# Performance work log

Measured on AMD Instinct MI355X. Metric: run time of the kernel, lower is better.

The kernel has to match this reference:

```python
import jax, jax.numpy as jnp
import numpy as np

N_NODES = 50000
N_EDGES = 800000
IN_DIM = 128
HID_DIM = 64


def gcn_conv(x, W, b, src, dst, ew):
    """PyG GCNConv with edge_weight: add self-loops (weight 1), symmetric
    normalization D^-1/2 (A+I) D^-1/2, linear transform, scatter-add, bias."""
    n = x.shape[0]
    loop = jnp.arange(n)
    src_a = jnp.concatenate([src, loop])           # [E+N]
    dst_a = jnp.concatenate([dst, loop])
    ew_a = jnp.concatenate([ew, jnp.ones((n,), dtype=x.dtype)])
    deg = jax.ops.segment_sum(ew_a, dst_a, num_segments=n)   # [N]
    dinv = jnp.where(deg > 0, jax.lax.rsqrt(deg), 0.0)
    norm = dinv[src_a] * ew_a * dinv[dst_a]        # [E+N]
    h = x @ W                                      # [N, out]
    msg = h[src_a] * norm[:, None]                 # gather + scale
    out = jax.ops.segment_sum(msg, dst_a, num_segments=n)    # scatter-add
    return out + b


def setup_inputs() -> dict:
    key = jax.random.key(0)
    k = jax.random.split(key, 6)
    x = jax.random.normal(k[0], (N_NODES, IN_DIM), dtype=jnp.float32)
    edge_index = jax.random.randint(k[1], (2, N_EDGES), 0, N_NODES, dtype=jnp.int64)
    edge_weight = jax.random.uniform(k[2], (N_EDGES,), dtype=jnp.float32)
    W1 = jax.random.normal(k[3], (IN_DIM, HID_DIM), dtype=jnp.float32) * (1.0 / np.sqrt(IN_DIM))
    b1 = jnp.zeros((HID_DIM,), dtype=jnp.float32)
    W2 = jax.random.normal(k[4], (HID_DIM, 1), dtype=jnp.float32) * (1.0 / np.sqrt(HID_DIM))
    b2 = jnp.zeros((1,), dtype=jnp.float32)
    return {"x": x, "edge_index": edge_index, "edge_weight": edge_weight,
            "W1": W1, "b1": b1, "W2": W2, "b2": b2}


def reference(x, edge_index, edge_weight, W1, b1, W2, b2):
    src, dst = edge_index[0], edge_index[1]
    h = gcn_conv(x, W1, b1, src, dst, edge_weight)
    h = jax.nn.relu(h)
    h = gcn_conv(h, W2, b2, src, dst, edge_weight)
    return jax.nn.sigmoid(h).squeeze(-1)           # [N]
```

## Files before the change

### kernel.cpp

```cpp
#include <hip/hip_runtime.h>
#include <hip/hip_bf16.h>
#include <math.h>

#define N_NODES 50000
#define N_EDGES 800000
#define IN_DIM  128
#define HID_DIM 64

#define NBKT     196
#define BKT_CAP  5000
#define NPASSC   200
#define EDGES_PER_PASSC (N_EDGES / NPASSC)
#define GEMM_NODES 64
#define NGEMM    782
#define XS_LD    132

__global__ __launch_bounds__(256)
void partgemm_kernel(const int* __restrict__ src, const int* __restrict__ dst,
                     const float* __restrict__ ew, int* __restrict__ gcursor,
                     int2* __restrict__ edge_b,
                     const float* __restrict__ x, const float* __restrict__ W1,
                     __hip_bfloat16* __restrict__ h1b) {
    __shared__ float w1s[IN_DIM * HID_DIM];
    __shared__ float xs[GEMM_NODES][XS_LD];
    int bid = blockIdx.x;
    int tid = threadIdx.x;
    if (bid < NPASSC) {
        int* cnt1    = (int*)w1s;
        int* cnt2    = cnt1 + NBKT;
        int* runbase = cnt2 + NBKT;
        if (tid < NBKT) { cnt1[tid] = 0; cnt2[tid] = 0; }
        __syncthreads();
        int e0 = bid * EDGES_PER_PASSC;
        for (int i = tid; i < EDGES_PER_PASSC; i += 256)
            atomicAdd(&cnt1[dst[e0 + i] >> 8], 1);
        __syncthreads();
        if (tid < NBKT) {
            int c = cnt1[tid];
            runbase[tid] = (c > 0) ? atomicAdd(&gcursor[tid], c) : 0;
        }
        __syncthreads();
        for (int i = tid; i < EDGES_PER_PASSC; i += 256) {
            int e = e0 + i;
            int d = dst[e];
            int b = d >> 8;
            int lr = atomicAdd(&cnt2[b], 1);
            int pos = b * BKT_CAP + runbase[b] + lr;
            edge_b[pos] = make_int2(src[e] | ((d & 255) << 16), __float_as_int(ew[e]));
        }
        return;
    }
    int gb = bid - NPASSC;
    int node0 = gb * GEMM_NODES;
    const float4* W4 = (const float4*)W1;
    float4* w1s4 = (float4*)w1s;
#pragma unroll
    for (int i = 0; i < 8; ++i) w1s4[tid + 256 * i] = W4[tid + 256 * i];
    {
        int r = tid >> 2, q = tid & 3;
        int row = node0 + r;
        if (row >= N_NODES) row = N_NODES - 1;
        const float4* xr = (const float4*)(x + (long)row * IN_DIM + q * 32);
#pragma unroll
        for (int i = 0; i < 8; ++i)
            *(float4*)&xs[r][q * 32 + i * 4] = xr[i];
    }
    __syncthreads();
    int w    = tid >> 6;
    int lane = tid & 63;
    int ng   = lane >> 2;
    int jg   = lane & 3;
    int j0   = w * 16 + jg * 4;
    float acc[4][4] = {{0.f}};
#pragma unroll 2
    for (int k = 0; k < IN_DIM; k += 4) {
        float4 wr0 = *(const float4*)&w1s[(k + 0) * HID_DIM + j0];
        float4 wr1 = *(const float4*)&w1s[(k + 1) * HID_DIM + j0];
        float4 wr2 = *(const float4*)&w1s[(k + 2) * HID_DIM + j0];
        float4 wr3 = *(const float4*)&w1s[(k + 3) * HID_DIM + j0];
#pragma unroll
        for (int i = 0; i < 4; ++i) {
            float4 xv = *(const float4*)&xs[ng + 16 * i][k];
            acc[i][0] += xv.x * wr0.x + xv.y * wr1.x + xv.z * wr2.x + xv.w * wr3.x;
            acc[i][1] += xv.x * wr0.y + xv.y * wr1.y + xv.z * wr2.y + xv.w * wr3.y;
            acc[i][2] += xv.x * wr0.z + xv.y * wr1.z + xv.z * wr2.z + xv.w * wr3.z;
            acc[i][3] += xv.x * wr0.w + xv.y * wr1.w + xv.z * wr2.w + xv.w * wr3.w;
        }
    }
#pragma unroll
    for (int i = 0; i < 4; ++i) {
        int n = node0 + ng + 16 * i;
        if (n < N_NODES) {
            __hip_bfloat16 bf[4];
            bf[0] = __float2bfloat16(acc[i][0]);
            bf[1] = __float2bfloat16(acc[i][1]);
            bf[2] = __float2bfloat16(acc[i][2]);
            bf[3] = __float2bfloat16(acc[i][3]);
            *(uint2*)&h1b[(long)n * HID_DIM + j0] = *(uint2*)bf;
        }
    }
}

__global__ __launch_bounds__(1024)
void bsort_kernel(const int* __restrict__ gcursor, const int2* __restrict__ edge_b,
                  int2* __restrict__ edge_s, int* __restrict__ start_g,
                  int* __restrict__ cnt_g, float* __restrict__ dinv) {
    __shared__ int   cnt[256];
    __shared__ int   cnt2[256];
    __shared__ float deg[256];
    __shared__ int   sc[256];
    int b   = blockIdx.x;
    int tid = threadIdx.x;
    int M    = gcursor[b];
    int base = b * BKT_CAP;
    if (tid < 256) { cnt[tid] = 0; cnt2[tid] = 0; deg[tid] = 0.0f; }
    __syncthreads();
    for (int i = tid; i < M; i += 1024) {
        int2 e = edge_b[base + i];
        int ld = (e.x >> 16) & 255;
        atomicAdd(&cnt[ld], 1);
        atomicAdd(&deg[ld], __int_as_float(e.y));
    }
    __syncthreads();
    if (tid < 256) sc[tid] = cnt[tid];
    __syncthreads();
#pragma unroll
    for (int off = 1; off < 256; off <<= 1) {
        int t = (tid >= off && tid < 256) ? sc[tid - off] : 0;
        __syncthreads();
        if (tid < 256) sc[tid] += t;
        __syncthreads();
    }
    if (tid < 256) {
        int startL = sc[tid] - cnt[tid];
        int node = b * 256 + tid;
        if (node < N_NODES) {
            start_g[node] = base + startL;
            cnt_g[node]   = cnt[tid];
            dinv[node]    = rsqrtf(1.0f + deg[tid]);
        }
        sc[tid] = startL;
    }
    __syncthreads();
    for (int i = tid; i < M; i += 1024) {
        int2 e = edge_b[base + i];
        int ld = (e.x >> 16) & 255;
        int r = atomicAdd(&cnt2[ld], 1);
        edge_s[base + sc[ld] + r] = make_int2(e.x & 0xFFFF, e.y);
    }
}

__global__ void gather1_layer2_kernel(const int* __restrict__ start_g, const int* __restrict__ cnt_g,
                                      const int2* __restrict__ edge_s,
                                      const __hip_bfloat16* __restrict__ h1b,
                                      const float* __restrict__ dinv, const float* __restrict__ b1,
                                      const float* __restrict__ W2, float* __restrict__ h2s) {
    __shared__ int2 meta[4][64];
    int wave = (blockIdx.x * blockDim.x + threadIdx.x) >> 6;
    int wl = threadIdx.x >> 6;
    int lane = threadIdx.x & 63;
    if (wave >= N_NODES) return;
    int s0 = start_g[wave];
    int ctotal = cnt_g[wave];
    int c0 = (lane & 31) * 2;
    int half = lane >> 5;
    float accA = 0.f, accB = 0.f;
    float accA2 = 0.f, accB2 = 0.f;
    for (int done = 0; done < ctotal; done += 64) {
        int cnt = ctotal - done;
        if (cnt > 64) cnt = 64;
        if (lane < cnt) {
            int2 m = edge_s[s0 + done + lane];
            float w = __int_as_float(m.y) * dinv[m.x];
            meta[wl][lane] = make_int2(m.x, __float_as_int(w));
        }
        __builtin_amdgcn_wave_barrier();
        int cnte = cnt & ~1;
        int j = 0;
        for (; j + 16 <= cnte; j += 16) {
            int2 m0 = meta[wl][j +  0 + half];
            int2 m1 = meta[wl][j +  2 + half];
            int2 m2 = meta[wl][j +  4 + half];
            int2 m3 = meta[wl][j +  6 + half];
            int2 m4 = meta[wl][j +  8 + half];
            int2 m5 = meta[wl][j + 10 + half];
            int2 m6 = meta[wl][j + 12 + half];
            int2 m7 = meta[wl][j + 14 + half];
            unsigned int p0 = *(const unsigned int*)&h1b[m0.x * HID_DIM + c0];
            unsigned int p1 = *(const unsigned int*)&h1b[m1.x * HID_DIM + c0];
            unsigned int p2 = *(const unsigned int*)&h1b[m2.x * HID_DIM + c0];
            unsigned int p3 = *(const unsigned int*)&h1b[m3.x * HID_DIM + c0];
            unsigned int p4 = *(const unsigned int*)&h1b[m4.x * HID_DIM + c0];
            unsigned int p5 = *(const unsigned int*)&h1b[m5.x * HID_DIM + c0];
            unsigned int p6 = *(const unsigned int*)&h1b[m6.x * HID_DIM + c0];
            unsigned int p7 = *(const unsigned int*)&h1b[m7.x * HID_DIM + c0];
            float w0 = __int_as_float(m0.y), w1 = __int_as_float(m1.y);
            float w2 = __int_as_float(m2.y), w3 = __int_as_float(m3.y);
            float w4 = __int_as_float(m4.y), w5 = __int_as_float(m5.y);
            float w6 = __int_as_float(m6.y), w7 = __int_as_float(m7.y);
            accA  += w0 * __uint_as_float(p0 << 16);
            accB  += w0 * __uint_as_float(p0 & 0xFFFF0000u);
            accA2 += w1 * __uint_as_float(p1 << 16);
            accB2 += w1 * __uint_as_float(p1 & 0xFFFF0000u);
            accA  += w2 * __uint_as_float(p2 << 16);
            accB  += w2 * __uint_as_float(p2 & 0xFFFF0000u);
            accA2 += w3 * __uint_as_float(p3 << 16);
            accB2 += w3 * __uint_as_float(p3 & 0xFFFF0000u);
            accA  += w4 * __uint_as_float(p4 << 16);
            accB  += w4 * __uint_as_float(p4 & 0xFFFF0000u);
            accA2 += w5 * __uint_as_float(p5 << 16);
            accB2 += w5 * __uint_as_float(p5 & 0xFFFF0000u);
            accA  += w6 * __uint_as_float(p6 << 16);
            accB  += w6 * __uint_as_float(p6 & 0xFFFF0000u);
            accA2 += w7 * __uint_as_float(p7 << 16);
            accB2 += w7 * __uint_as_float(p7 & 0xFFFF0000u);
        }
        for (; j + 2 <= cnte; j += 2) {
            int2 m = meta[wl][j + half];
            unsigned int p = *(const unsigned int*)&h1b[m.x * HID_DIM + c0];
            accA += __int_as_float(m.y) * __uint_as_float(p << 16);
            accB += __int_as_float(m.y) * __uint_as_float(p & 0xFFFF0000u);
        }
        if (cnt & 1) {
            if (half == 0) {
                int2 m = meta[wl][cnt - 1];
                unsigned int p = *(const unsigned int*)&h1b[m.x * HID_DIM + c0];
                accA += __int_as_float(m.y) * __uint_as_float(p << 16);
                accB += __int_as_float(m.y) * __uint_as_float(p & 0xFFFF0000u);
            }
        }
        __builtin_amdgcn_wave_barrier();
    }
    accA += accA2; accB += accB2;
    accA += __shfl_xor(accA, 32, 64);
    accB += __shfl_xor(accB, 32, 64);
    float di = dinv[wave];
    unsigned int sp = *(const unsigned int*)&h1b[wave * HID_DIM + c0];
    float s0f = __uint_as_float(sp << 16);
    float s1f = __uint_as_float(sp & 0xFFFF0000u);
    float z0 = di * (accA + di * s0f) + b1[c0];
    float z1 = di * (accB + di * s1f) + b1[c0 + 1];
    float h0 = fmaxf(z0, 0.0f);
    float h1v = fmaxf(z1, 0.0f);
    float v = h0 * W2[c0] + h1v * W2[c0 + 1];
#pragma unroll
    for (int off = 16; off > 0; off >>= 1)
        v += __shfl_down(v, off, 32);
    if (lane == 0) h2s[wave] = v * di;
}

__global__ void gather2_final_kernel(const int* __restrict__ start_g, const int* __restrict__ cnt_g,
                                     const int2* __restrict__ edge_s,
                                     const float* __restrict__ h2s, const float* __restrict__ dinv,
                                     const float* __restrict__ b2, float* __restrict__ out) {
    int t = blockIdx.x * blockDim.x + threadIdx.x;
    int n = t >> 4;
    int sub = t & 15;
    if (n >= N_NODES) return;
    int s0 = start_g[n];
    int cnt = cnt_g[n];
    float acc = 0.0f;
    for (int j = sub; j < cnt; j += 16) {
        int2 m = edge_s[s0 + j];
        acc += __int_as_float(m.y) * h2s[m.x];
    }
#pragma unroll
    for (int off = 8; off > 0; off >>= 1)
        acc += __shfl_down(acc, off, 16);
    if (sub == 0) {
        float z = dinv[n] * (acc + h2s[n]) + b2[0];
        out[n] = 1.0f / (1.0f + expf(-z));
    }
}

extern "C" void kernel_launch(void* const* d_in, const int* in_sizes, int n_in,
                              void* d_out, int out_size, void* d_ws, size_t ws_size,
                              hipStream_t stream) {
    const float* x  = (const float*)d_in[0];
    const int*   ei = (const int*)d_in[1];
    const float* ew = (const float*)d_in[2];
    const float* W1 = (const float*)d_in[3];
    const float* b1 = (const float*)d_in[4];
    const float* W2 = (const float*)d_in[5];
    const float* b2 = (const float*)d_in[6];
    float* out = (float*)d_out;

    const int* src = ei;
    const int* dst = ei + N_EDGES;

    char* ws = (char*)d_ws;
    int2*  edge_b  = (int2*)ws;              ws += (size_t)NBKT * BKT_CAP * sizeof(int2);
    int2*  edge_s  = (int2*)ws;              ws += (size_t)NBKT * BKT_CAP * sizeof(int2);
    int*   gcursor = (int*)ws;               ws += NBKT * sizeof(int);
    int*   start_g = (int*)ws;               ws += N_NODES * sizeof(int);
    int*   cnt_g   = (int*)ws;               ws += N_NODES * sizeof(int);
    float* dinv    = (float*)ws;             ws += N_NODES * sizeof(float);
    float* h2s     = (float*)ws;             ws += N_NODES * sizeof(float);
    ws = (char*)(((uintptr_t)ws + 127) & ~(uintptr_t)127);
    __hip_bfloat16* h1b = (__hip_bfloat16*)ws;

    hipMemsetAsync(gcursor, 0, NBKT * sizeof(int), stream);
    partgemm_kernel<<<NPASSC + NGEMM, 256, 0, stream>>>(src, dst, ew, gcursor, edge_b, x, W1, h1b);
    bsort_kernel<<<NBKT, 1024, 0, stream>>>(gcursor, edge_b, edge_s, start_g, cnt_g, dinv);
    gather1_layer2_kernel<<<(N_NODES * 64) / 256, 256, 0, stream>>>(start_g, cnt_g, edge_s, h1b, dinv, b1, W2, h2s);
    gather2_final_kernel<<<(N_NODES * 16 + 255) / 256, 256, 0, stream>>>(start_g, cnt_g, edge_s, h2s, dinv, b2, out);
}
```

Measured before the change: 155.1 us.

## Fuse bucket sort and both gathers into one cooperative persistent kernel

Replaces three kernel launches (bucket sort, layer-1 gather plus layer-2 transform, final gather) with one cooperative kernel that separates the phases with grid-wide syncs. The grid is persistent and capped by occupancy, so gather work is distributed with grid-stride loops. The aim is to remove launch gaps and kernel-boundary drains. In exchange the sort phase now runs with 256 threads per block instead of 1024, grid syncs add their own cost, and the fixed grid of 1024 blocks may give lower parallelism for the gather phases than the former large launches.

New measurement: 376.8 us. 143% more time.

```diff
diff --git a/kernel.cpp b/kernel.cpp
--- a/kernel.cpp
+++ b/kernel.cpp
@@ -1,6 +1,9 @@
 #include <hip/hip_runtime.h>
 #include <hip/hip_bf16.h>
+#include <hip/hip_cooperative_groups.h>
 #include <math.h>
+
+namespace cg = cooperative_groups;
 
 #define N_NODES 50000
 #define N_EDGES 800000
@@ -14,6 +17,7 @@
 #define GEMM_NODES 64
 #define NGEMM    782
 #define XS_LD    132
+#define GRID_FUSED 1024
 
 __global__ __launch_bounds__(256)
 void partgemm_kernel(const int* __restrict__ src, const int* __restrict__ dst,
@@ -101,175 +105,175 @@
     }
 }
 
-__global__ __launch_bounds__(1024)
-void bsort_kernel(const int* __restrict__ gcursor, const int2* __restrict__ edge_b,
-                  int2* __restrict__ edge_s, int* __restrict__ start_g,
-                  int* __restrict__ cnt_g, float* __restrict__ dinv) {
+__global__ __launch_bounds__(256, 4)
+void fused_post_kernel(const int* __restrict__ gcursor, const int2* __restrict__ edge_b,
+                       int2* __restrict__ edge_s, int* __restrict__ start_g,
+                       int* __restrict__ cnt_g, float* __restrict__ dinv,
+                       const __hip_bfloat16* __restrict__ h1b,
+                       const float* __restrict__ b1, const float* __restrict__ W2,
+                       float* __restrict__ h2s, const float* __restrict__ b2,
+                       float* __restrict__ out) {
+    cg::grid_group grid = cg::this_grid();
     __shared__ int   cnt[256];
     __shared__ int   cnt2[256];
     __shared__ float deg[256];
     __shared__ int   sc[256];
-    int b   = blockIdx.x;
+    __shared__ int2  meta[4][64];
     int tid = threadIdx.x;
-    int M    = gcursor[b];
-    int base = b * BKT_CAP;
-    if (tid < 256) { cnt[tid] = 0; cnt2[tid] = 0; deg[tid] = 0.0f; }
-    __syncthreads();
-    for (int i = tid; i < M; i += 1024) {
-        int2 e = edge_b[base + i];
-        int ld = (e.x >> 16) & 255;
-        atomicAdd(&cnt[ld], 1);
-        atomicAdd(&deg[ld], __int_as_float(e.y));
-    }
-    __syncthreads();
-    if (tid < 256) sc[tid] = cnt[tid];
-    __syncthreads();
-#pragma unroll
-    for (int off = 1; off < 256; off <<= 1) {
-        int t = (tid >= off && tid < 256) ? sc[tid - off] : 0;
-        __syncthreads();
-        if (tid < 256) sc[tid] += t;
-        __syncthreads();
-    }
-    if (tid < 256) {
+    int bid = blockIdx.x;
+    int gthread  = bid * 256 + tid;
+    int nthreads = gridDim.x * 256;
+
+    if (bid < NBKT) {
+        int M    = gcursor[bid];
+        int base = bid * BKT_CAP;
+        cnt[tid] = 0; cnt2[tid] = 0; deg[tid] = 0.0f;
+        __syncthreads();
+        for (int i = tid; i < M; i += 256) {
+            int2 e = edge_b[base + i];
+            int ld = (e.x >> 16) & 255;
+            atomicAdd(&cnt[ld], 1);
+            atomicAdd(&deg[ld], __int_as_float(e.y));
+        }
+        __syncthreads();
+        sc[tid] = cnt[tid];
+        __syncthreads();
+#pragma unroll
+        for (int off = 1; off < 256; off <<= 1) {
+            int t = (tid >= off) ? sc[tid - off] : 0;
+            __syncthreads();
+            sc[tid] += t;
+            __syncthreads();
+        }
         int startL = sc[tid] - cnt[tid];
-        int node = b * 256 + tid;
+        int node = bid * 256 + tid;
         if (node < N_NODES) {
             start_g[node] = base + startL;
             cnt_g[node]   = cnt[tid];
             dinv[node]    = rsqrtf(1.0f + deg[tid]);
         }
         sc[tid] = startL;
-    }
-    __syncthreads();
-    for (int i = tid; i < M; i += 1024) {
-        int2 e = edge_b[base + i];
-        int ld = (e.x >> 16) & 255;
-        int r = atomicAdd(&cnt2[ld], 1);
-        edge_s[base + sc[ld] + r] = make_int2(e.x & 0xFFFF, e.y);
-    }
-}
-
-__global__ void gather1_layer2_kernel(const int* __restrict__ start_g, const int* __restrict__ cnt_g,
-                                      const int2* __restrict__ edge_s,
-                                      const __hip_bfloat16* __restrict__ h1b,
-                                      const float* __restrict__ dinv, const float* __restrict__ b1,
-                                      const float* __restrict__ W2, float* __restrict__ h2s) {
-    __shared__ int2 meta[4][64];
-    int wave = (blockIdx.x * blockDim.x + threadIdx.x) >> 6;
-    int wl = threadIdx.x >> 6;
-    int lane = threadIdx.x & 63;
-    if (wave >= N_NODES) return;
-    int s0 = start_g[wave];
-    int ctotal = cnt_g[wave];
-    int c0 = (lane & 31) * 2;
-    int half = lane >> 5;
-    float accA = 0.f, accB = 0.f;
-    float accA2 = 0.f, accB2 = 0.f;
-    for (int done = 0; done < ctotal; done += 64) {
-        int cnt = ctotal - done;
-        if (cnt > 64) cnt = 64;
-        if (lane < cnt) {
-            int2 m = edge_s[s0 + done + lane];
-            float w = __int_as_float(m.y) * dinv[m.x];
-            meta[wl][lane] = make_int2(m.x, __float_as_int(w));
-        }
-        __builtin_amdgcn_wave_barrier();
-        int cnte = cnt & ~1;
-        int j = 0;
-        for (; j + 16 <= cnte; j += 16) {
-            int2 m0 = meta[wl][j +  0 + half];
-            int2 m1 = meta[wl][j +  2 + half];
-            int2 m2 = meta[wl][j +  4 + half];
-            int2 m3 = meta[wl][j +  6 + half];
-            int2 m4 = meta[wl][j +  8 + half];
-            int2 m5 = meta[wl][j + 10 + half];
-            int2 m6 = meta[wl][j + 12 + half];
-            int2 m7 = meta[wl][j + 14 + half];
-            unsigned int p0 = *(const unsigned int*)&h1b[m0.x * HID_DIM + c0];
-            unsigned int p1 = *(const unsigned int*)&h1b[m1.x * HID_DIM + c0];
-            unsigned int p2 = *(const unsigned int*)&h1b[m2.x * HID_DIM + c0];
-            unsigned int p3 = *(const unsigned int*)&h1b[m3.x * HID_DIM + c0];
-            unsigned int p4 = *(const unsigned int*)&h1b[m4.x * HID_DIM + c0];
-            unsigned int p5 = *(const unsigned int*)&h1b[m5.x * HID_DIM + c0];
-            unsigned int p6 = *(const unsigned int*)&h1b[m6.x * HID_DIM + c0];
-            unsigned int p7 = *(const unsigned int*)&h1b[m7.x * HID_DIM + c0];
-            float w0 = __int_as_float(m0.y), w1 = __int_as_float(m1.y);
-            float w2 = __int_as_float(m2.y), w3 = __int_as_float(m3.y);
-            float w4 = __int_as_float(m4.y), w5 = __int_as_float(m5.y);
-            float w6 = __int_as_float(m6.y), w7 = __int_as_float(m7.y);
-            accA  += w0 * __uint_as_float(p0 << 16);
-            accB  += w0 * __uint_as_float(p0 & 0xFFFF0000u);
-            accA2 += w1 * __uint_as_float(p1 << 16);
-            accB2 += w1 * __uint_as_float(p1 & 0xFFFF0000u);
-            accA  += w2 * __uint_as_float(p2 << 16);
-            accB  += w2 * __uint_as_float(p2 & 0xFFFF0000u);
-            accA2 += w3 * __uint_as_float(p3 << 16);
-            accB2 += w3 * __uint_as_float(p3 & 0xFFFF0000u);
-            accA  += w4 * __uint_as_float(p4 << 16);
-            accB  += w4 * __uint_as_float(p4 & 0xFFFF0000u);
-            accA2 += w5 * __uint_as_float(p5 << 16);
-            accB2 += w5 * __uint_as_float(p5 & 0xFFFF0000u);
-            accA  += w6 * __uint_as_float(p6 << 16);
-            accB  += w6 * __uint_as_float(p6 & 0xFFFF0000u);
-            accA2 += w7 * __uint_as_float(p7 << 16);
-            accB2 += w7 * __uint_as_float(p7 & 0xFFFF0000u);
-        }
-        for (; j + 2 <= cnte; j += 2) {
-            int2 m = meta[wl][j + half];
-            unsigned int p = *(const unsigned int*)&h1b[m.x * HID_DIM + c0];
-            accA += __int_as_float(m.y) * __uint_as_float(p << 16);
-            accB += __int_as_float(m.y) * __uint_as_float(p & 0xFFFF0000u);
-        }
-        if (cnt & 1) {
-            if (half == 0) {
-                int2 m = meta[wl][cnt - 1];
-                unsigned int p = *(const unsigned int*)&h1b[m.x * HID_DIM + c0];
-                accA += __int_as_float(m.y) * __uint_as_float(p << 16);
-                accB += __int_as_float(m.y) * __uint_as_float(p & 0xFFFF0000u);
+        __syncthreads();
+        for (int i = tid; i < M; i += 256) {
+            int2 e = edge_b[base + i];
+            int ld = (e.x >> 16) & 255;
+            int r = atomicAdd(&cnt2[ld], 1);
+            edge_s[base + sc[ld] + r] = make_int2(e.x & 0xFFFF, e.y);
+        }
+    }
+    grid.sync();
+
+    {
+        int wl   = tid >> 6;
+        int lane = tid & 63;
+        int gwave    = gthread >> 6;
+        int totWaves = nthreads >> 6;
+        int c0   = (lane & 31) * 2;
+        int half = lane >> 5;
+        for (int node = gwave; node < N_NODES; node += totWaves) {
+            int s0 = start_g[node];
+            int ctotal = cnt_g[node];
+            float accA = 0.f, accB = 0.f, accA2 = 0.f, accB2 = 0.f;
+            for (int done = 0; done < ctotal; done += 64) {
+                int cnt_ = ctotal - done;
+                if (cnt_ > 64) cnt_ = 64;
+                if (lane < cnt_) {
+                    int2 m = edge_s[s0 + done + lane];
+                    float w = __int_as_float(m.y) * dinv[m.x];
+                    meta[wl][lane] = make_int2(m.x, __float_as_int(w));
+                }
+                __builtin_amdgcn_wave_barrier();
+                int cnte = cnt_ & ~1;
+                int j = 0;
+                for (; j + 16 <= cnte; j += 16) {
+                    int2 m0 = meta[wl][j +  0 + half];
+                    int2 m1 = meta[wl][j +  2 + half];
+                    int2 m2 = meta[wl][j +  4 + half];
+                    int2 m3 = meta[wl][j +  6 + half];
+                    int2 m4 = meta[wl][j +  8 + half];
+                    int2 m5 = meta[wl][j + 10 + half];
+                    int2 m6 = meta[wl][j + 12 + half];
+                    int2 m7 = meta[wl][j + 14 + half];
+                    unsigned int p0 = *(const unsigned int*)&h1b[m0.x * HID_DIM + c0];
+                    unsigned int p1 = *(const unsigned int*)&h1b[m1.x * HID_DIM + c0];
+                    unsigned int p2 = *(const unsigned int*)&h1b[m2.x * HID_DIM + c0];
+                    unsigned int p3 = *(const unsigned int*)&h1b[m3.x * HID_DIM + c0];
+                    unsigned int p4 = *(const unsigned int*)&h1b[m4.x * HID_DIM + c0];
+                    unsigned int p5 = *(const unsigned int*)&h1b[m5.x * HID_DIM + c0];
+                    unsigned int p6 = *(const unsigned int*)&h1b[m6.x * HID_DIM + c0];
+                    unsigned int p7 = *(const unsigned int*)&h1b[m7.x * HID_DIM + c0];
+                    float w0 = __int_as_float(m0.y), w1 = __int_as_float(m1.y);
+                    float w2 = __int_as_float(m2.y), w3 = __int_as_float(m3.y);
+                    float w4 = __int_as_float(m4.y), w5 = __int_as_float(m5.y);
+                    float w6 = __int_as_float(m6.y), w7 = __int_as_float(m7.y);
+                    accA  += w0 * __uint_as_float(p0 << 16);
+                    accB  += w0 * __uint_as_float(p0 & 0xFFFF0000u);
+                    accA2 += w1 * __uint_as_float(p1 << 16);
+                    accB2 += w1 * __uint_as_float(p1 & 0xFFFF0000u);
+                    accA  += w2 * __uint_as_float(p2 << 16);
+                    accB  += w2 * __uint_as_float(p2 & 0xFFFF0000u);
+                    accA2 += w3 * __uint_as_float(p3 << 16);
+                    accB2 += w3 * __uint_as_float(p3 & 0xFFFF0000u);
+                    accA  += w4 * __uint_as_float(p4 << 16);
+                    accB  += w4 * __uint_as_float(p4 & 0xFFFF0000u);
+                    accA2 += w5 * __uint_as_float(p5 << 16);
+                    accB2 += w5 * __uint_as_float(p5 & 0xFFFF0000u);
+                    accA  += w6 * __uint_as_float(p6 << 16);
+                    accB  += w6 * __uint_as_float(p6 & 0xFFFF0000u);
+                    accA2 += w7 * __uint_as_float(p7 << 16);
+                    accB2 += w7 * __uint_as_float(p7 & 0xFFFF0000u);
+                }
+                for (; j + 2 <= cnte; j += 2) {
+                    int2 m = meta[wl][j + half];
+                    unsigned int p = *(const unsigned int*)&h1b[m.x * HID_DIM + c0];
+                    accA += __int_as_float(m.y) * __uint_as_float(p << 16);
+                    accB += __int_as_float(m.y) * __uint_as_float(p & 0xFFFF0000u);
+                }
+                if ((cnt_ & 1) && half == 0) {
+                    int2 m = meta[wl][cnt_ - 1];
+                    unsigned int p = *(const unsigned int*)&h1b[m.x * HID_DIM + c0];
+                    accA += __int_as_float(m.y) * __uint_as_float(p << 16);
+                    accB += __int_as_float(m.y) * __uint_as_float(p & 0xFFFF0000u);
+                }
+                __builtin_amdgcn_wave_barrier();
             }
-        }
-        __builtin_amdgcn_wave_barrier();
-    }
-    accA += accA2; accB += accB2;
-    accA += __shfl_xor(accA, 32, 64);
-    accB += __shfl_xor(accB, 32, 64);
-    float di = dinv[wave];
-    unsigned int sp = *(const unsigned int*)&h1b[wave * HID_DIM + c0];
-    float s0f = __uint_as_float(sp << 16);
-    float s1f = __uint_as_float(sp & 0xFFFF0000u);
-    float z0 = di * (accA + di * s0f) + b1[c0];
-    float z1 = di * (accB + di * s1f) + b1[c0 + 1];
-    float h0 = fmaxf(z0, 0.0f);
-    float h1v = fmaxf(z1, 0.0f);
-    float v = h0 * W2[c0] + h1v * W2[c0 + 1];
-#pragma unroll
-    for (int off = 16; off > 0; off >>= 1)
-        v += __shfl_down(v, off, 32);
-    if (lane == 0) h2s[wave] = v * di;
-}
-
-__global__ void gather2_final_kernel(const int* __restrict__ start_g, const int* __restrict__ cnt_g,
-                                     const int2* __restrict__ edge_s,
-                                     const float* __restrict__ h2s, const float* __restrict__ dinv,
-                                     const float* __restrict__ b2, float* __restrict__ out) {
-    int t = blockIdx.x * blockDim.x + threadIdx.x;
-    int n = t >> 4;
-    int sub = t & 15;
-    if (n >= N_NODES) return;
-    int s0 = start_g[n];
-    int cnt = cnt_g[n];
-    float acc = 0.0f;
-    for (int j = sub; j < cnt; j += 16) {
-        int2 m = edge_s[s0 + j];
-        acc += __int_as_float(m.y) * h2s[m.x];
-    }
-#pragma unroll
-    for (int off = 8; off > 0; off >>= 1)
-        acc += __shfl_down(acc, off, 16);
-    if (sub == 0) {
-        float z = dinv[n] * (acc + h2s[n]) + b2[0];
-        out[n] = 1.0f / (1.0f + expf(-z));
+            accA += accA2; accB += accB2;
+            accA += __shfl_xor(accA, 32, 64);
+            accB += __shfl_xor(accB, 32, 64);
+            float di = dinv[node];
+            unsigned int sp = *(const unsigned int*)&h1b[(long)node * HID_DIM + c0];
+            float s0f = __uint_as_float(sp << 16);
+            float s1f = __uint_as_float(sp & 0xFFFF0000u);
+            float z0 = di * (accA + di * s0f) + b1[c0];
+            float z1 = di * (accB + di * s1f) + b1[c0 + 1];
+            float h0  = fmaxf(z0, 0.0f);
+            float h1v = fmaxf(z1, 0.0f);
+            float v = h0 * W2[c0] + h1v * W2[c0 + 1];
+#pragma unroll
+            for (int off = 16; off > 0; off >>= 1)
+                v += __shfl_down(v, off, 32);
+            if (lane == 0) h2s[node] = v * di;
+        }
+    }
+    grid.sync();
+
+    for (int t = gthread; t < N_NODES * 16; t += nthreads) {
+        int n = t >> 4;
+        int sub = t & 15;
+        int s0 = start_g[n];
+        int cnt_ = cnt_g[n];
+        float acc = 0.0f;
+        for (int j = sub; j < cnt_; j += 16) {
+            int2 m = edge_s[s0 + j];
+            acc += __int_as_float(m.y) * h2s[m.x];
+        }
+#pragma unroll
+        for (int off = 8; off > 0; off >>= 1)
+            acc += __shfl_down(acc, off, 16);
+        if (sub == 0) {
+            float z = dinv[n] * (acc + h2s[n]) + b2[0];
+            out[n] = 1.0f / (1.0f + expf(-z));
+        }
     }
 }
 
@@ -299,9 +303,21 @@
     ws = (char*)(((uintptr_t)ws + 127) & ~(uintptr_t)127);
     __hip_bfloat16* h1b = (__hip_bfloat16*)ws;
 
+    int grid_fused = GRID_FUSED;
+    {
+        int blocksPerCU = 0;
+        if (hipOccupancyMaxActiveBlocksPerMultiprocessor(&blocksPerCU,
+                (const void*)fused_post_kernel, 256, 0) == hipSuccess && blocksPerCU > 0) {
+            int cap = blocksPerCU * 256;
+            if (grid_fused > cap) grid_fused = cap;
+        }
+    }
+
     hipMemsetAsync(gcursor, 0, NBKT * sizeof(int), stream);
     partgemm_kernel<<<NPASSC + NGEMM, 256, 0, stream>>>(src, dst, ew, gcursor, edge_b, x, W1, h1b);
-    bsort_kernel<<<NBKT, 1024, 0, stream>>>(gcursor, edge_b, edge_s, start_g, cnt_g, dinv);
-    gather1_layer2_kernel<<<(N_NODES * 64) / 256, 256, 0, stream>>>(start_g, cnt_g, edge_s, h1b, dinv, b1, W2, h2s);
-    gather2_final_kernel<<<(N_NODES * 16 + 255) / 256, 256, 0, stream>>>(start_g, cnt_g, edge_s, h2s, dinv, b2, out);
+    void* params[] = {(void*)&gcursor, (void*)&edge_b, (void*)&edge_s,
+                      (void*)&start_g, (void*)&cnt_g, (void*)&dinv, (void*)&h1b,
+                      (void*)&b1, (void*)&W2, (void*)&h2s, (void*)&b2, (void*)&out};
+    hipLaunchCooperativeKernel((void*)fused_post_kernel, dim3(grid_fused), dim3(256),
+                               params, 0, stream);
 }
```

## Replace global bucket cursor atomics with per-pass local partitioning and fragment lookup

Applied to the files above, without the earlier changes.

The partition pass no longer reserves space in each global bucket with atomics. Each pass block now runs a local prefix scan and writes its edges contiguously into its own slice of edge_b, recording per-bucket counts and offsets in 2D tables. bsort scans those per-pass counts and binary-searches the fragment table to locate each edge, which also removes the hipMemsetAsync launch. In exchange, bsort's reads are split into up to 200 scattered fragments per bucket and each edge read pays a binary search.

Measured after the change: 158.4 us. +2.1%, slower.

```diff
diff --git a/kernel.cpp b/kernel.cpp
--- a/kernel.cpp
+++ b/kernel.cpp
@@ -17,7 +17,8 @@
 
 __global__ __launch_bounds__(256)
 void partgemm_kernel(const int* __restrict__ src, const int* __restrict__ dst,
-                     const float* __restrict__ ew, int* __restrict__ gcursor,
+                     const float* __restrict__ ew,
+                     int* __restrict__ cnt2d, int* __restrict__ off2d,
                      int2* __restrict__ edge_b,
                      const float* __restrict__ x, const float* __restrict__ W1,
                      __hip_bfloat16* __restrict__ h1b) {
@@ -26,18 +27,30 @@
     int bid = blockIdx.x;
     int tid = threadIdx.x;
     if (bid < NPASSC) {
-        int* cnt1    = (int*)w1s;
-        int* cnt2    = cnt1 + NBKT;
-        int* runbase = cnt2 + NBKT;
-        if (tid < NBKT) { cnt1[tid] = 0; cnt2[tid] = 0; }
+        int* cnt1   = (int*)w1s;
+        int* cnt2   = cnt1 + 256;
+        int* runoff = cnt2 + 256;
+        int* scuf   = runoff + 256;
+        cnt1[tid] = 0; cnt2[tid] = 0;
         __syncthreads();
         int e0 = bid * EDGES_PER_PASSC;
         for (int i = tid; i < EDGES_PER_PASSC; i += 256)
             atomicAdd(&cnt1[dst[e0 + i] >> 8], 1);
         __syncthreads();
+        scuf[tid] = cnt1[tid];
+        __syncthreads();
+#pragma unroll
+        for (int off = 1; off < 256; off <<= 1) {
+            int t = (tid >= off) ? scuf[tid - off] : 0;
+            __syncthreads();
+            scuf[tid] += t;
+            __syncthreads();
+        }
+        int excl = scuf[tid] - cnt1[tid];
         if (tid < NBKT) {
-            int c = cnt1[tid];
-            runbase[tid] = (c > 0) ? atomicAdd(&gcursor[tid], c) : 0;
+            runoff[tid] = excl;
+            cnt2d[bid * NBKT + tid] = cnt1[tid];
+            off2d[bid * NBKT + tid] = excl;
         }
         __syncthreads();
         for (int i = tid; i < EDGES_PER_PASSC; i += 256) {
@@ -45,7 +58,7 @@
             int d = dst[e];
             int b = d >> 8;
             int lr = atomicAdd(&cnt2[b], 1);
-            int pos = b * BKT_CAP + runbase[b] + lr;
+            int pos = bid * EDGES_PER_PASSC + runoff[b] + lr;
             edge_b[pos] = make_int2(src[e] | ((d & 255) << 16), __float_as_int(ew[e]));
         }
         return;
@@ -102,21 +115,42 @@
 }
 
 __global__ __launch_bounds__(1024)
-void bsort_kernel(const int* __restrict__ gcursor, const int2* __restrict__ edge_b,
+void bsort_kernel(const int* __restrict__ cnt2d, const int* __restrict__ off2d,
+                  const int2* __restrict__ edge_b,
                   int2* __restrict__ edge_s, int* __restrict__ start_g,
                   int* __restrict__ cnt_g, float* __restrict__ dinv) {
     __shared__ int   cnt[256];
     __shared__ int   cnt2[256];
     __shared__ float deg[256];
     __shared__ int   sc[256];
+    __shared__ int   fragbase[NPASSC + 1];
+    __shared__ int   fragoff[NPASSC];
     int b   = blockIdx.x;
     int tid = threadIdx.x;
-    int M    = gcursor[b];
     int base = b * BKT_CAP;
     if (tid < 256) { cnt[tid] = 0; cnt2[tid] = 0; deg[tid] = 0.0f; }
-    __syncthreads();
+    int fc = 0;
+    if (tid < NPASSC) {
+        fc = cnt2d[tid * NBKT + b];
+        fragoff[tid] = off2d[tid * NBKT + b];
+    }
+    if (tid < 256) sc[tid] = fc;
+    __syncthreads();
+#pragma unroll
+    for (int off = 1; off < 256; off <<= 1) {
+        int t = (tid >= off && tid < 256) ? sc[tid - off] : 0;
+        __syncthreads();
+        if (tid < 256) sc[tid] += t;
+        __syncthreads();
+    }
+    if (tid < NPASSC) fragbase[tid] = sc[tid] - fc;
+    if (tid == NPASSC - 1) fragbase[NPASSC] = sc[tid];
+    __syncthreads();
+    int M = fragbase[NPASSC];
     for (int i = tid; i < M; i += 1024) {
-        int2 e = edge_b[base + i];
+        int lo = 0, hi = NPASSC - 1;
+        while (lo < hi) { int mid = (lo + hi + 1) >> 1; if (fragbase[mid] <= i) lo = mid; else hi = mid - 1; }
+        int2 e = edge_b[lo * EDGES_PER_PASSC + fragoff[lo] + (i - fragbase[lo])];
         int ld = (e.x >> 16) & 255;
         atomicAdd(&cnt[ld], 1);
         atomicAdd(&deg[ld], __int_as_float(e.y));
@@ -143,7 +177,9 @@
     }
     __syncthreads();
     for (int i = tid; i < M; i += 1024) {
-        int2 e = edge_b[base + i];
+        int lo = 0, hi = NPASSC - 1;
+        while (lo < hi) { int mid = (lo + hi + 1) >> 1; if (fragbase[mid] <= i) lo = mid; else hi = mid - 1; }
+        int2 e = edge_b[lo * EDGES_PER_PASSC + fragoff[lo] + (i - fragbase[lo])];
         int ld = (e.x >> 16) & 255;
         int r = atomicAdd(&cnt2[ld], 1);
         edge_s[base + sc[ld] + r] = make_int2(e.x & 0xFFFF, e.y);
@@ -164,8 +200,7 @@
     int ctotal = cnt_g[wave];
     int c0 = (lane & 31) * 2;
     int half = lane >> 5;
-    float accA = 0.f, accB = 0.f;
-    float accA2 = 0.f, accB2 = 0.f;
+    float accA = 0.f, accB = 0.f, accA2 = 0.f, accB2 = 0.f;
     for (int done = 0; done < ctotal; done += 64) {
         int cnt = ctotal - done;
         if (cnt > 64) cnt = 64;
@@ -221,13 +256,11 @@
             accA += __int_as_float(m.y) * __uint_as_float(p << 16);
             accB += __int_as_float(m.y) * __uint_as_float(p & 0xFFFF0000u);
         }
-        if (cnt & 1) {
-            if (half == 0) {
-                int2 m = meta[wl][cnt - 1];
-                unsigned int p = *(const unsigned int*)&h1b[m.x * HID_DIM + c0];
-                accA += __int_as_float(m.y) * __uint_as_float(p << 16);
-                accB += __int_as_float(m.y) * __uint_as_float(p & 0xFFFF0000u);
-            }
+        if ((cnt & 1) && half == 0) {
+            int2 m = meta[wl][cnt - 1];
+            unsigned int p = *(const unsigned int*)&h1b[m.x * HID_DIM + c0];
+            accA += __int_as_float(m.y) * __uint_as_float(p << 16);
+            accB += __int_as_float(m.y) * __uint_as_float(p & 0xFFFF0000u);
         }
         __builtin_amdgcn_wave_barrier();
     }
@@ -240,7 +273,7 @@
     float s1f = __uint_as_float(sp & 0xFFFF0000u);
     float z0 = di * (accA + di * s0f) + b1[c0];
     float z1 = di * (accB + di * s1f) + b1[c0 + 1];
-    float h0 = fmaxf(z0, 0.0f);
+    float h0  = fmaxf(z0, 0.0f);
     float h1v = fmaxf(z1, 0.0f);
     float v = h0 * W2[c0] + h1v * W2[c0 + 1];
 #pragma unroll
@@ -289,9 +322,10 @@
     const int* dst = ei + N_EDGES;
 
     char* ws = (char*)d_ws;
-    int2*  edge_b  = (int2*)ws;              ws += (size_t)NBKT * BKT_CAP * sizeof(int2);
+    int2*  edge_b  = (int2*)ws;              ws += (size_t)N_EDGES * sizeof(int2);
     int2*  edge_s  = (int2*)ws;              ws += (size_t)NBKT * BKT_CAP * sizeof(int2);
-    int*   gcursor = (int*)ws;               ws += NBKT * sizeof(int);
+    int*   cnt2d   = (int*)ws;               ws += (size_t)NPASSC * NBKT * sizeof(int);
+    int*   off2d   = (int*)ws;               ws += (size_t)NPASSC * NBKT * sizeof(int);
     int*   start_g = (int*)ws;               ws += N_NODES * sizeof(int);
     int*   cnt_g   = (int*)ws;               ws += N_NODES * sizeof(int);
     float* dinv    = (float*)ws;             ws += N_NODES * sizeof(float);
@@ -299,9 +333,8 @@
     ws = (char*)(((uintptr_t)ws + 127) & ~(uintptr_t)127);
     __hip_bfloat16* h1b = (__hip_bfloat16*)ws;
 
-    hipMemsetAsync(gcursor, 0, NBKT * sizeof(int), stream);
-    partgemm_kernel<<<NPASSC + NGEMM, 256, 0, stream>>>(src, dst, ew, gcursor, edge_b, x, W1, h1b);
-    bsort_kernel<<<NBKT, 1024, 0, stream>>>(gcursor, edge_b, edge_s, start_g, cnt_g, dinv);
+    partgemm_kernel<<<NPASSC + NGEMM, 256, 0, stream>>>(src, dst, ew, cnt2d, off2d, edge_b, x, W1, h1b);
+    bsort_kernel<<<NBKT, 1024, 0, stream>>>(cnt2d, off2d, edge_b, edge_s, start_g, cnt_g, dinv);
     gather1_layer2_kernel<<<(N_NODES * 64) / 256, 256, 0, stream>>>(start_g, cnt_g, edge_s, h1b, dinv, b1, W2, h2s);
     gather2_final_kernel<<<(N_NODES * 16 + 255) / 256, 256, 0, stream>>>(start_g, cnt_g, edge_s, h2s, dinv, b2, out);
 }
```
